# Kernel tuning notes

Hardware: AMD Instinct MI355X
Metric: run time of the kernel (lower is better)

## Reference

```python
import jax, jax.numpy as jnp
import numpy as np

SEQ_LEN = 2048
EMBED_DIM = 1024
NUM_HEADS = 16
DIM_HEAD = EMBED_DIM // NUM_HEADS
BATCH = 4


def setup_inputs() -> dict:
    key = jax.random.key(0)
    k1, k2, k3 = jax.random.split(key, 3)
    x = jax.random.normal(k1, (SEQ_LEN, BATCH, EMBED_DIM), dtype=jnp.float32)
    weight_qkv = jax.random.normal(k2, (3 * EMBED_DIM, EMBED_DIM), dtype=jnp.float32) * (EMBED_DIM ** -0.5)
    weight_out = jax.random.normal(k3, (EMBED_DIM, EMBED_DIM), dtype=jnp.float32) * (EMBED_DIM ** -0.5)
    # causal mask: True where attention is DISALLOWED (strict upper triangle)
    mask = ~jnp.tril(jnp.ones((SEQ_LEN, SEQ_LEN), dtype=bool))[None, None]  # [1,1,L,L]
    return {"x": x, "weight_qkv": weight_qkv, "weight_out": weight_out, "mask": mask}


def reference(x, weight_qkv, weight_out, mask):
    L, N, E = x.shape
    H, Dh = NUM_HEADS, DIM_HEAD
    scale = Dh ** -0.5
    qkv = x @ weight_qkv.T                       # [L, N, 3E]
    q, k, v = jnp.split(qkv, 3, axis=-1)         # each [L, N, E]
    # [L, N, E] -> [N*H, L, Dh]
    def to_heads(t):
        return t.reshape(L, N * H, Dh).transpose(1, 0, 2)
    q, k, v = to_heads(q) * scale, to_heads(k), to_heads(v)
    attn = jnp.einsum('bld,bmd->blm', q, k)      # [N*H, L, L]
    attn = attn.reshape(N, H, L, L)
    attn = jnp.where(mask, jnp.float32(-100000.0), attn)
    attn = jax.nn.softmax(attn.reshape(N * H, L, L), axis=-1)
    out = jnp.einsum('blm,bmd->bld', attn, v)    # [N*H, L, Dh]
    out = out.transpose(1, 0, 2).reshape(L, N, E)
    return out @ weight_out.T
```

## Files before the change

kernel.cpp:

```cpp
#include <hip/hip_runtime.h>
#include <hip/hip_bf16.h>
#include <stdint.h>

constexpr int L  = 2048;
constexpr int NB = 4;
constexpr int E  = 1024;
constexpr int H  = 16;
constexpr int M  = L * NB;
constexpr int K  = E;
constexpr int QKV_LD = 3 * E;

typedef float  f32x4  __attribute__((ext_vector_type(4)));
typedef __bf16 bf16x4 __attribute__((ext_vector_type(4)));
typedef __bf16 bf16x8 __attribute__((ext_vector_type(8)));

#define AS1 __attribute__((address_space(1)))
#define AS3 __attribute__((address_space(3)))

static __device__ __forceinline__ void gl_lds16(const void* g, void* l) {
  __builtin_amdgcn_global_load_lds((const AS1 uint32_t*)g, (AS3 uint32_t*)l, 16, 0, 0);
}

__global__ __launch_bounds__(256)
void cvt_f32_bf16(const float* __restrict__ in, __bf16* __restrict__ out, int n4) {
  const int i = blockIdx.x * blockDim.x + threadIdx.x;
  if (i < n4) {
    const f32x4 v = ((const f32x4*)in)[i];
    bf16x4 o;
#pragma unroll
    for (int j = 0; j < 4; j++) o[j] = (__bf16)v[j];
    ((bf16x4*)out)[i] = o;
  }
}

template<int NC, typename OutT>
__global__ __launch_bounds__(256)
void gemm_bt(const __bf16* __restrict__ A, const __bf16* __restrict__ B,
             OutT* __restrict__ C) {
  constexpr int BK = 64;
  __shared__ char lds[2 * 128 * BK * 2];
  char* aL = lds;
  char* bL = lds + 128 * BK * 2;

  const int t    = threadIdx.x;
  const int lane = t & 63;
  const int w    = t >> 6;
  const int g    = lane >> 4;
  const int c    = lane & 15;

  const int nwg = gridDim.x * gridDim.y;
  const int lin = blockIdx.x + gridDim.x * blockIdx.y;
  const int q8  = nwg >> 3;
  const int swz = (lin & 7) * q8 + (lin >> 3);
  const int bx  = swz % gridDim.x;
  const int by  = swz / gridDim.x;

  const int rowBase = by * 128;
  const int colBase = bx * 128;

  const int srow = t >> 3;
  const int scb  = (t & 7) * 16;
  const int ssw  = scb ^ ((srow & 7) << 4);

  const char* aSrcBase = (const char*)(A + (size_t)(rowBase + srow) * K) + ssw;
  const char* bSrcBase = (const char*)(B + (size_t)(colBase + srow) * K) + ssw;

  f32x4 acc[4][4];
#pragma unroll
  for (int i = 0; i < 4; i++)
#pragma unroll
    for (int j = 0; j < 4; j++) acc[i][j] = f32x4{0.f, 0.f, 0.f, 0.f};

  const int wr = (w >> 1) * 64;
  const int wc = (w & 1) * 64;

  for (int k0 = 0; k0 < K; k0 += BK) {
    __syncthreads();
#pragma unroll
    for (int q = 0; q < 4; q++) {
      gl_lds16(aSrcBase + (size_t)2 * k0 + (size_t)q * 32 * K * 2, aL + q * 4096 + t * 16);
      gl_lds16(bSrcBase + (size_t)2 * k0 + (size_t)q * 32 * K * 2, bL + q * 4096 + t * 16);
    }
    __syncthreads();

    bf16x8 af[4][2], bfR[4][2];
#pragma unroll
    for (int mi = 0; mi < 4; mi++) {
      const int row = wr + mi * 16 + c;
      const int sw  = (row & 7) << 4;
#pragma unroll
      for (int ks = 0; ks < 2; ks++)
        af[mi][ks] = *(const bf16x8*)(aL + row * 128 + ((ks * 64 + g * 16) ^ sw));
    }
#pragma unroll
    for (int ni = 0; ni < 4; ni++) {
      const int row = wc + ni * 16 + c;
      const int sw  = (row & 7) << 4;
#pragma unroll
      for (int ks = 0; ks < 2; ks++)
        bfR[ni][ks] = *(const bf16x8*)(bL + row * 128 + ((ks * 64 + g * 16) ^ sw));
    }
#pragma unroll
    for (int mi = 0; mi < 4; mi++)
#pragma unroll
      for (int ni = 0; ni < 4; ni++)
#pragma unroll
        for (int ks = 0; ks < 2; ks++)
          acc[mi][ni] = __builtin_amdgcn_mfma_f32_16x16x32_bf16(
              af[mi][ks], bfR[ni][ks], acc[mi][ni], 0, 0, 0);
  }

#pragma unroll
  for (int mi = 0; mi < 4; mi++)
#pragma unroll
    for (int ni = 0; ni < 4; ni++)
#pragma unroll
      for (int r = 0; r < 4; r++) {
        const int row = rowBase + wr + mi * 16 + g * 4 + r;
        const int col = colBase + wc + ni * 16 + c;
        C[(size_t)row * NC + col] = (OutT)acc[mi][ni][r];
      }
}

__global__ __launch_bounds__(256)
void transpose_v(const __bf16* __restrict__ qkv, __bf16* __restrict__ vT) {
  __shared__ char tile[64 * 160];
  const int lt = blockIdx.x;
  const int bh = blockIdx.y;
  const int n  = bh >> 4, h = bh & 15;
  const int t  = threadIdx.x;
  const int r8 = t >> 3;
  const int c8 = (t & 7) * 8;

#pragma unroll
  for (int q2 = 0; q2 < 2; q2++) {
    const int l = q2 * 32 + r8;
    const bf16x8 v = *(const bf16x8*)(qkv + (size_t)((lt * 64 + l) * 4 + n) * QKV_LD +
                                      2 * E + h * 64 + c8);
    *(bf16x8*)(tile + l * 160 + ((c8 * 2) ^ (((l >> 3) & 7) << 4))) = v;
  }
  __syncthreads();
#pragma unroll
  for (int q2 = 0; q2 < 2; q2++) {
    const int d = q2 * 32 + r8;
    bf16x8 o;
#pragma unroll
    for (int i = 0; i < 8; i++) {
      const int l = c8 + i;
      o[i] = *(const __bf16*)(tile + l * 160 + ((d * 2) ^ (((l >> 3) & 7) << 4)));
    }
    *(bf16x8*)(vT + ((size_t)bh * 64 + d) * 2048 + lt * 64 + c8) = o;
  }
}

__global__ __launch_bounds__(256)
void attn_kernel(const __bf16* __restrict__ qkv, const __bf16* __restrict__ vT,
                 __bf16* __restrict__ out) {
  const int b  = blockIdx.x;
  const int qx = blockIdx.y;
  const int n  = b >> 4;
  const int h  = b & 15;

  __shared__ char kl[2][64 * 128];
  __shared__ char vl[2][64 * 128];
  __shared__ char pl[4][16 * 128];

  const int t    = threadIdx.x;
  const int lane = t & 63;
  const int w    = t >> 6;
  const int g    = lane >> 4;
  const int c    = lane & 15;

  const int srow = t >> 3;
  const int scb  = (t & 7) * 16;
  const int kssw = scb ^ ((srow & 7) << 4);

  constexpr float QSCALE = 0.125f * 1.4426950408889634f;

  char* pw = pl[w];
  const int qloc = w * 16 + c;

  int cur = 0;

  for (int pass = 0; pass < 2; ++pass) {
    const int qt = pass ? 31 - qx : qx;

    bf16x8 qa0, qa1;
    {
      const int qrow = qt * 64 + qloc;
      const __bf16* qp = qkv + (size_t)(qrow * 4 + n) * QKV_LD + h * 64;
      qa0 = *(const bf16x8*)(qp + g * 8);
      qa1 = *(const bf16x8*)(qp + 32 + g * 8);
#pragma unroll
      for (int i = 0; i < 8; i++) {
        qa0[i] = (__bf16)((float)qa0[i] * QSCALE);
        qa1[i] = (__bf16)((float)qa1[i] * QSCALE);
      }
    }

    float m_c = -3e38f, l_c = 0.f;
    f32x4 o[4];
#pragma unroll
    for (int ni = 0; ni < 4; ni++) o[ni] = f32x4{0.f, 0.f, 0.f, 0.f};

    if (pass == 0) {
#pragma unroll
      for (int q2 = 0; q2 < 2; q2++) {
        const int kvrow = q2 * 32 + srow;
        gl_lds16((const char*)(qkv + (size_t)(kvrow * 4 + n) * QKV_LD + E + h * 64) + kssw,
                 kl[cur] + q2 * 4096 + t * 16);
        gl_lds16((const char*)(vT + ((size_t)b * 64 + q2 * 32 + srow) * 2048) + kssw,
                 vl[cur] + q2 * 4096 + t * 16);
      }
    }

    for (int kt = 0; kt <= qt; ++kt) {
      __syncthreads();

      const bool lastTile = (kt == qt);
      if (!lastTile || pass == 0) {
        const int nx = lastTile ? 0 : kt + 1;
#pragma unroll
        for (int q2 = 0; q2 < 2; q2++) {
          const int kvrow = nx * 64 + q2 * 32 + srow;
          gl_lds16((const char*)(qkv + (size_t)(kvrow * 4 + n) * QKV_LD + E + h * 64) + kssw,
                   kl[cur ^ 1] + q2 * 4096 + t * 16);
          const int vd = q2 * 32 + srow;
          gl_lds16((const char*)(vT + ((size_t)b * 64 + vd) * 2048 + nx * 64) + kssw,
                   vl[cur ^ 1] + q2 * 4096 + t * 16);
        }
      }
      __builtin_amdgcn_sched_barrier(0);

      const char* klc = kl[cur];
      const char* vlc = vl[cur];

      f32x4 s[4];
#pragma unroll
      for (int ni = 0; ni < 4; ni++) s[ni] = f32x4{0.f, 0.f, 0.f, 0.f};
      __builtin_amdgcn_s_setprio(1);
#pragma unroll
      for (int ni = 0; ni < 4; ni++) {
        const int row = ni * 16 + c;
        const int sw  = (row & 7) << 4;
        const bf16x8 kb0 = *(const bf16x8*)(klc + row * 128 + ((g * 16) ^ sw));
        const bf16x8 kb1 = *(const bf16x8*)(klc + row * 128 + ((64 + g * 16) ^ sw));
        s[ni] = __builtin_amdgcn_mfma_f32_16x16x32_bf16(kb0, qa0, s[ni], 0, 0, 0);
        s[ni] = __builtin_amdgcn_mfma_f32_16x16x32_bf16(kb1, qa1, s[ni], 0, 0, 0);
      }
      __builtin_amdgcn_s_setprio(0);

      if (lastTile) {
#pragma unroll
        for (int ni = 0; ni < 4; ni++)
#pragma unroll
          for (int r = 0; r < 4; r++)
            if (ni * 16 + g * 4 + r > qloc) s[ni][r] = -3e38f;
      }

      float rmax = -3e38f;
#pragma unroll
      for (int ni = 0; ni < 4; ni++)
#pragma unroll
        for (int r = 0; r < 4; r++) rmax = fmaxf(rmax, s[ni][r]);
      rmax = fmaxf(rmax, __shfl_xor(rmax, 16));
      rmax = fmaxf(rmax, __shfl_xor(rmax, 32));

      if (__any(rmax > m_c + 8.f)) {
        const float mnew  = fmaxf(m_c, rmax);
        const float alpha = exp2f(m_c - mnew);
        l_c *= alpha;
#pragma unroll
        for (int r = 0; r < 4; r++) {
          const float ar = __shfl(alpha, g * 4 + r);
#pragma unroll
          for (int ni = 0; ni < 4; ni++) o[ni][r] *= ar;
        }
        m_c = mnew;
      }

      float rsum = 0.f;
#pragma unroll
      for (int ni = 0; ni < 4; ni++)
#pragma unroll
        for (int r = 0; r < 4; r++) {
          const float e = exp2f(s[ni][r] - m_c);
          s[ni][r] = e;
          rsum += e;
        }
      rsum += __shfl_xor(rsum, 16);
      rsum += __shfl_xor(rsum, 32);
      l_c += rsum;

#pragma unroll
      for (int ni = 0; ni < 4; ni++) {
        bf16x4 pk;
#pragma unroll
        for (int r = 0; r < 4; r++) pk[r] = (__bf16)s[ni][r];
        *(bf16x4*)(pw + c * 128 + ((ni * 32 + g * 8) ^ ((c & 7) << 4))) = pk;
      }
      bf16x8 pa[2];
      {
        const int sw = (c & 7) << 4;
        pa[0] = *(const bf16x8*)(pw + c * 128 + ((g * 16) ^ sw));
        pa[1] = *(const bf16x8*)(pw + c * 128 + ((64 + g * 16) ^ sw));
      }
      __builtin_amdgcn_s_setprio(1);
#pragma unroll
      for (int ni = 0; ni < 4; ni++) {
        const int row = ni * 16 + c;
        const int sw  = (row & 7) << 4;
        const bf16x8 vb0 = *(const bf16x8*)(vlc + row * 128 + ((g * 16) ^ sw));
        const bf16x8 vb1 = *(const bf16x8*)(vlc + row * 128 + ((64 + g * 16) ^ sw));
        o[ni] = __builtin_amdgcn_mfma_f32_16x16x32_bf16(pa[0], vb0, o[ni], 0, 0, 0);
        o[ni] = __builtin_amdgcn_mfma_f32_16x16x32_bf16(pa[1], vb1, o[ni], 0, 0, 0);
      }
      __builtin_amdgcn_s_setprio(0);

      cur ^= 1;
    }

#pragma unroll
    for (int r = 0; r < 4; r++) {
      const float lr   = __shfl(l_c, g * 4 + r);
      const float inv  = 1.f / lr;
      const int   qrow = qt * 64 + w * 16 + g * 4 + r;
#pragma unroll
      for (int ni = 0; ni < 4; ni++) {
        const size_t off = (size_t)(qrow * 4 + n) * E + h * 64 + ni * 16 + c;
        out[off] = (__bf16)(o[ni][r] * inv);
      }
    }
  }
}

extern "C" void kernel_launch(void* const* d_in, const int* in_sizes, int n_in,
                              void* d_out, int out_size, void* d_ws, size_t ws_size,
                              hipStream_t stream) {
  const float* x    = (const float*)d_in[0];
  const float* wqkv = (const float*)d_in[1];
  const float* wout = (const float*)d_in[2];

  char* ws = (char*)d_ws;
  __bf16* x_bf    = (__bf16*)ws;                         ws += (size_t)M * E * 2;
  __bf16* wqkv_bf = (__bf16*)ws;                         ws += (size_t)QKV_LD * E * 2;
  __bf16* wout_bf = (__bf16*)ws;                         ws += (size_t)E * E * 2;
  __bf16* qkv     = (__bf16*)ws;                         ws += (size_t)M * QKV_LD * 2;
  __bf16* attno   = (__bf16*)ws;
  __bf16* vT      = x_bf;
  float*  outp    = (float*)d_out;

  cvt_f32_bf16<<<(M * E / 4) / 256, 256, 0, stream>>>(x, x_bf, M * E / 4);
  cvt_f32_bf16<<<(QKV_LD * E / 4) / 256, 256, 0, stream>>>(wqkv, wqkv_bf, QKV_LD * E / 4);
  cvt_f32_bf16<<<(E * E / 4) / 256, 256, 0, stream>>>(wout, wout_bf, E * E / 4);

  gemm_bt<QKV_LD, __bf16><<<dim3(QKV_LD / 128, M / 128), 256, 0, stream>>>(x_bf, wqkv_bf, qkv);
  transpose_v<<<dim3(L / 64, NB * H), 256, 0, stream>>>(qkv, vT);
  attn_kernel<<<dim3(NB * H, 16), 256, 0, stream>>>(qkv, vT, attno);
  gemm_bt<E, float><<<dim3(E / 128, M / 128), 256, 0, stream>>>(attno, wout_bf, outp);
}
```

Before: 196.0 us.

## Switch attention to 32x32x16 MFMA and co-schedule paired query tiles across waves

The attention kernel now uses 32x32x16 bf16 MFMA tiles, with each wave owning 32 query rows instead of 16. Previously a block ran two query tiles in sequential passes. Now two waves handle tile qx and two handle tile 31-qx concurrently, sharing one K/V stream up to the longer tile's end. This removes the second pass's reload and serialization and gives larger MFMA shapes with fewer LDS reads per flop. In exchange, waves on the short tile sit idle for part of the loop, register pressure rises from 16-wide accumulators, and the LDS swizzle is changed.

```diff
diff --git a/kernel.cpp b/kernel.cpp
--- a/kernel.cpp
+++ b/kernel.cpp
@@ -11,6 +11,7 @@
 constexpr int QKV_LD = 3 * E;
 
 typedef float  f32x4  __attribute__((ext_vector_type(4)));
+typedef float  f32x16 __attribute__((ext_vector_type(16)));
 typedef __bf16 bf16x4 __attribute__((ext_vector_type(4)));
 typedef __bf16 bf16x8 __attribute__((ext_vector_type(8)));
 
@@ -163,107 +164,111 @@
 
   __shared__ char kl[2][64 * 128];
   __shared__ char vl[2][64 * 128];
-  __shared__ char pl[4][16 * 128];
+  __shared__ char pl[4][32 * 128];
 
   const int t    = threadIdx.x;
   const int lane = t & 63;
   const int w    = t >> 6;
-  const int g    = lane >> 4;
-  const int c    = lane & 15;
+  const int l31  = lane & 31;
+  const int hi   = lane >> 5;
 
   const int srow = t >> 3;
   const int scb  = (t & 7) * 16;
-  const int kssw = scb ^ ((srow & 7) << 4);
+  int kssw[2];
+#pragma unroll
+  for (int q2 = 0; q2 < 2; q2++) {
+    const int row = q2 * 32 + srow;
+    kssw[q2] = scb ^ (((row ^ (row >> 3)) & 7) << 4);
+  }
+
+  const int krow0 = l31,      sw0 = ((krow0 ^ (krow0 >> 3)) & 7) << 4;
+  const int krow1 = 32 + l31, sw1 = ((krow1 ^ (krow1 >> 3)) & 7) << 4;
 
   constexpr float QSCALE = 0.125f * 1.4426950408889634f;
 
+  const int qt    = (w < 2) ? qx : 31 - qx;
+  const int qh    = w & 1;
+  const int ktEnd = 31 - qx;
+  const int qg    = qt * 64 + qh * 32 + l31;
+
   char* pw = pl[w];
-  const int qloc = w * 16 + c;
+
+  bf16x8 qb[4];
+  {
+    const __bf16* qp = qkv + (size_t)(qg * 4 + n) * QKV_LD + h * 64;
+#pragma unroll
+    for (int ds = 0; ds < 4; ds++) {
+      qb[ds] = *(const bf16x8*)(qp + ds * 16 + hi * 8);
+#pragma unroll
+      for (int i = 0; i < 8; i++) qb[ds][i] = (__bf16)((float)qb[ds][i] * QSCALE);
+    }
+  }
+
+  float m_c = -3e38f, l_c = 0.f;
+  f32x16 o0, o1;
+#pragma unroll
+  for (int j = 0; j < 16; j++) { o0[j] = 0.f; o1[j] = 0.f; }
 
   int cur = 0;
 
-  for (int pass = 0; pass < 2; ++pass) {
-    const int qt = pass ? 31 - qx : qx;
-
-    bf16x8 qa0, qa1;
-    {
-      const int qrow = qt * 64 + qloc;
-      const __bf16* qp = qkv + (size_t)(qrow * 4 + n) * QKV_LD + h * 64;
-      qa0 = *(const bf16x8*)(qp + g * 8);
-      qa1 = *(const bf16x8*)(qp + 32 + g * 8);
-#pragma unroll
-      for (int i = 0; i < 8; i++) {
-        qa0[i] = (__bf16)((float)qa0[i] * QSCALE);
-        qa1[i] = (__bf16)((float)qa1[i] * QSCALE);
-      }
-    }
-
-    float m_c = -3e38f, l_c = 0.f;
-    f32x4 o[4];
-#pragma unroll
-    for (int ni = 0; ni < 4; ni++) o[ni] = f32x4{0.f, 0.f, 0.f, 0.f};
-
-    if (pass == 0) {
+#pragma unroll
+  for (int q2 = 0; q2 < 2; q2++) {
+    const int kvrow = q2 * 32 + srow;
+    gl_lds16((const char*)(qkv + (size_t)(kvrow * 4 + n) * QKV_LD + E + h * 64) + kssw[q2],
+             kl[0] + q2 * 4096 + t * 16);
+    gl_lds16((const char*)(vT + ((size_t)b * 64 + kvrow) * 2048) + kssw[q2],
+             vl[0] + q2 * 4096 + t * 16);
+  }
+
+  for (int kt = 0; kt <= ktEnd; ++kt) {
+    __syncthreads();
+
+    if (kt < ktEnd) {
+      const int nx = kt + 1;
 #pragma unroll
       for (int q2 = 0; q2 < 2; q2++) {
-        const int kvrow = q2 * 32 + srow;
-        gl_lds16((const char*)(qkv + (size_t)(kvrow * 4 + n) * QKV_LD + E + h * 64) + kssw,
-                 kl[cur] + q2 * 4096 + t * 16);
-        gl_lds16((const char*)(vT + ((size_t)b * 64 + q2 * 32 + srow) * 2048) + kssw,
-                 vl[cur] + q2 * 4096 + t * 16);
-      }
-    }
-
-    for (int kt = 0; kt <= qt; ++kt) {
-      __syncthreads();
-
-      const bool lastTile = (kt == qt);
-      if (!lastTile || pass == 0) {
-        const int nx = lastTile ? 0 : kt + 1;
-#pragma unroll
-        for (int q2 = 0; q2 < 2; q2++) {
-          const int kvrow = nx * 64 + q2 * 32 + srow;
-          gl_lds16((const char*)(qkv + (size_t)(kvrow * 4 + n) * QKV_LD + E + h * 64) + kssw,
-                   kl[cur ^ 1] + q2 * 4096 + t * 16);
-          const int vd = q2 * 32 + srow;
-          gl_lds16((const char*)(vT + ((size_t)b * 64 + vd) * 2048 + nx * 64) + kssw,
-                   vl[cur ^ 1] + q2 * 4096 + t * 16);
-        }
-      }
-      __builtin_amdgcn_sched_barrier(0);
-
+        const int kvrow = nx * 64 + q2 * 32 + srow;
+        gl_lds16((const char*)(qkv + (size_t)(kvrow * 4 + n) * QKV_LD + E + h * 64) + kssw[q2],
+                 kl[cur ^ 1] + q2 * 4096 + t * 16);
+        const int vd = q2 * 32 + srow;
+        gl_lds16((const char*)(vT + ((size_t)b * 64 + vd) * 2048 + nx * 64) + kssw[q2],
+                 vl[cur ^ 1] + q2 * 4096 + t * 16);
+      }
+    }
+    __builtin_amdgcn_sched_barrier(0);
+
+    if (kt <= qt) {
       const char* klc = kl[cur];
       const char* vlc = vl[cur];
 
-      f32x4 s[4];
-#pragma unroll
-      for (int ni = 0; ni < 4; ni++) s[ni] = f32x4{0.f, 0.f, 0.f, 0.f};
+      f32x16 s0, s1;
+#pragma unroll
+      for (int j = 0; j < 16; j++) { s0[j] = 0.f; s1[j] = 0.f; }
       __builtin_amdgcn_s_setprio(1);
 #pragma unroll
-      for (int ni = 0; ni < 4; ni++) {
-        const int row = ni * 16 + c;
-        const int sw  = (row & 7) << 4;
-        const bf16x8 kb0 = *(const bf16x8*)(klc + row * 128 + ((g * 16) ^ sw));
-        const bf16x8 kb1 = *(const bf16x8*)(klc + row * 128 + ((64 + g * 16) ^ sw));
-        s[ni] = __builtin_amdgcn_mfma_f32_16x16x32_bf16(kb0, qa0, s[ni], 0, 0, 0);
-        s[ni] = __builtin_amdgcn_mfma_f32_16x16x32_bf16(kb1, qa1, s[ni], 0, 0, 0);
+      for (int ds = 0; ds < 4; ds++) {
+        const int col = ds * 32 + hi * 16;
+        const bf16x8 ka0 = *(const bf16x8*)(klc + krow0 * 128 + (col ^ sw0));
+        const bf16x8 ka1 = *(const bf16x8*)(klc + krow1 * 128 + (col ^ sw1));
+        s0 = __builtin_amdgcn_mfma_f32_32x32x16_bf16(ka0, qb[ds], s0, 0, 0, 0);
+        s1 = __builtin_amdgcn_mfma_f32_32x32x16_bf16(ka1, qb[ds], s1, 0, 0, 0);
       }
       __builtin_amdgcn_s_setprio(0);
 
-      if (lastTile) {
-#pragma unroll
-        for (int ni = 0; ni < 4; ni++)
-#pragma unroll
-          for (int r = 0; r < 4; r++)
-            if (ni * 16 + g * 4 + r > qloc) s[ni][r] = -3e38f;
-      }
-
-      float rmax = -3e38f;
-#pragma unroll
-      for (int ni = 0; ni < 4; ni++)
-#pragma unroll
-        for (int r = 0; r < 4; r++) rmax = fmaxf(rmax, s[ni][r]);
-      rmax = fmaxf(rmax, __shfl_xor(rmax, 16));
+      if (kt == qt) {
+#pragma unroll
+        for (int reg = 0; reg < 16; reg++) {
+          const int kvp = (reg & 3) + 8 * (reg >> 2) + 4 * hi;
+          if (kt * 64 + kvp      > qg) s0[reg] = -1e30f;
+          if (kt * 64 + 32 + kvp > qg) s1[reg] = -1e30f;
+        }
+      }
+
+      float rmax = s0[0];
+#pragma unroll
+      for (int reg = 1; reg < 16; reg++) rmax = fmaxf(rmax, s0[reg]);
+#pragma unroll
+      for (int reg = 0; reg < 16; reg++) rmax = fmaxf(rmax, s1[reg]);
       rmax = fmaxf(rmax, __shfl_xor(rmax, 32));
 
       if (__any(rmax > m_c + 8.f)) {
@@ -271,66 +276,61 @@
         const float alpha = exp2f(m_c - mnew);
         l_c *= alpha;
 #pragma unroll
-        for (int r = 0; r < 4; r++) {
-          const float ar = __shfl(alpha, g * 4 + r);
-#pragma unroll
-          for (int ni = 0; ni < 4; ni++) o[ni][r] *= ar;
+        for (int reg = 0; reg < 16; reg++) {
+          const int   qp = (reg & 3) + 8 * (reg >> 2) + 4 * hi;
+          const float ar = __shfl(alpha, qp);
+          o0[reg] *= ar;
+          o1[reg] *= ar;
         }
         m_c = mnew;
       }
 
       float rsum = 0.f;
 #pragma unroll
-      for (int ni = 0; ni < 4; ni++)
-#pragma unroll
-        for (int r = 0; r < 4; r++) {
-          const float e = exp2f(s[ni][r] - m_c);
-          s[ni][r] = e;
-          rsum += e;
-        }
-      rsum += __shfl_xor(rsum, 16);
+      for (int reg = 0; reg < 16; reg++) {
+        const float e0 = exp2f(s0[reg] - m_c);
+        const float e1 = exp2f(s1[reg] - m_c);
+        s0[reg] = e0; s1[reg] = e1;
+        rsum += e0 + e1;
+      }
       rsum += __shfl_xor(rsum, 32);
       l_c += rsum;
 
 #pragma unroll
-      for (int ni = 0; ni < 4; ni++) {
+      for (int rg = 0; rg < 8; rg++) {
         bf16x4 pk;
 #pragma unroll
-        for (int r = 0; r < 4; r++) pk[r] = (__bf16)s[ni][r];
-        *(bf16x4*)(pw + c * 128 + ((ni * 32 + g * 8) ^ ((c & 7) << 4))) = pk;
-      }
-      bf16x8 pa[2];
-      {
-        const int sw = (c & 7) << 4;
-        pa[0] = *(const bf16x8*)(pw + c * 128 + ((g * 16) ^ sw));
-        pa[1] = *(const bf16x8*)(pw + c * 128 + ((64 + g * 16) ^ sw));
-      }
-      __builtin_amdgcn_s_setprio(1);
-#pragma unroll
-      for (int ni = 0; ni < 4; ni++) {
-        const int row = ni * 16 + c;
-        const int sw  = (row & 7) << 4;
-        const bf16x8 vb0 = *(const bf16x8*)(vlc + row * 128 + ((g * 16) ^ sw));
-        const bf16x8 vb1 = *(const bf16x8*)(vlc + row * 128 + ((64 + g * 16) ^ sw));
-        o[ni] = __builtin_amdgcn_mfma_f32_16x16x32_bf16(pa[0], vb0, o[ni], 0, 0, 0);
-        o[ni] = __builtin_amdgcn_mfma_f32_16x16x32_bf16(pa[1], vb1, o[ni], 0, 0, 0);
-      }
-      __builtin_amdgcn_s_setprio(0);
-
-      cur ^= 1;
-    }
-
-#pragma unroll
-    for (int r = 0; r < 4; r++) {
-      const float lr   = __shfl(l_c, g * 4 + r);
-      const float inv  = 1.f / lr;
-      const int   qrow = qt * 64 + w * 16 + g * 4 + r;
-#pragma unroll
-      for (int ni = 0; ni < 4; ni++) {
-        const size_t off = (size_t)(qrow * 4 + n) * E + h * 64 + ni * 16 + c;
-        out[off] = (__bf16)(o[ni][r] * inv);
-      }
-    }
+        for (int j = 0; j < 4; j++)
+          pk[j] = (__bf16)((rg < 4) ? s0[(rg & 3) * 4 + j] : s1[(rg & 3) * 4 + j]);
+        const int kvb = (rg & 3) * 16 + hi * 8 + (rg >> 2) * 64;
+        *(bf16x4*)(pw + l31 * 128 + (kvb ^ sw0)) = pk;
+      }
+
+#pragma unroll
+      for (int s_ = 0; s_ < 4; s_++) {
+        const int colp = s_ * 32 + hi * 16;
+        const bf16x8 pa  = *(const bf16x8*)(pw + l31 * 128 + (colp ^ sw0));
+        const bf16x8 vb0 = *(const bf16x8*)(vlc + krow0 * 128 + (colp ^ sw0));
+        const bf16x8 vb1 = *(const bf16x8*)(vlc + krow1 * 128 + (colp ^ sw1));
+        __builtin_amdgcn_s_setprio(1);
+        o0 = __builtin_amdgcn_mfma_f32_32x32x16_bf16(pa, vb0, o0, 0, 0, 0);
+        o1 = __builtin_amdgcn_mfma_f32_32x32x16_bf16(pa, vb1, o1, 0, 0, 0);
+        __builtin_amdgcn_s_setprio(0);
+      }
+    }
+
+    cur ^= 1;
+  }
+
+  const float inv = 1.f / l_c;
+#pragma unroll
+  for (int reg = 0; reg < 16; reg++) {
+    const int   qp  = (reg & 3) + 8 * (reg >> 2) + 4 * hi;
+    const float li  = __shfl(inv, qp);
+    const int   qrw = qt * 64 + qh * 32 + qp;
+    const size_t base = (size_t)(qrw * 4 + n) * E + h * 64;
+    out[base + l31]      = (__bf16)(o0[reg] * li);
+    out[base + 32 + l31] = (__bf16)(o1[reg] * li);
   }
 }
 
```

After: 218.9 us. 1.12x slower.
